# Optimization experiments

Hardware: AMD Instinct MI355X
Metric: run time of the kernel (lower is better)

The kernel has to match this reference:

```python
import jax, jax.numpy as jnp
import numpy as np

N_ATOMS = 16384
N_BLOCKS = 4096
K = 3          # top-k nearest context atoms (min(3, n_ctx) in original; n_ctx >> 3 here)
EPS_W = 1e-8   # inverse-distance weight epsilon (matches original)
EPS_D = 1e-12  # tiny epsilon inside sqrt for numerical safety of the distance


def setup_inputs() -> dict:
    key = jax.random.key(0)
    k1, k2, k3, k4, k5 = jax.random.split(key, 5)
    # coordinates spread out like real molecular coords (Angstrom-ish scale)
    X = jax.random.normal(k1, (N_ATOMS, 3), dtype=jnp.float32) * 10.0
    base_noise = jax.random.normal(k2, (N_ATOMS, 3), dtype=jnp.float32)      # randn_like(X)
    centroid_noise = jax.random.normal(k3, (N_ATOMS, 3), dtype=jnp.float32)  # per-atom randn(3)
    block_ids = jnp.sort(jax.random.randint(k4, (N_ATOMS,), 0, N_BLOCKS)).astype(jnp.int32)
    generate_mask = jax.random.randint(k5, (N_BLOCKS,), 0, 2).astype(bool)
    return {
        "X": X,
        "base_noise": base_noise,
        "centroid_noise": centroid_noise,
        "block_ids": block_ids,
        "generate_mask": generate_mask,
    }


def reference(X, base_noise, centroid_noise, block_ids, generate_mask):
    """Vectorized sample_chemical_prior: for every generated atom, find the 3
    nearest CONTEXT atoms, take an inverse-distance-weighted centroid, and add
    0.5 * gaussian noise. Non-generated atoms keep base_noise (randn_like)."""
    n = X.shape[0]
    gen_atoms = generate_mask[block_ids]           # [N] atoms being generated
    ctx = ~gen_atoms                               # [N] context atoms

    # pairwise squared distances via ||a||^2 + ||b||^2 - 2 a.b  -> [N, N]
    xn = jnp.sum(X * X, axis=-1)
    sq = xn[:, None] + xn[None, :] - 2.0 * (X @ X.T)
    d = jnp.sqrt(jnp.maximum(sq, 0.0) + EPS_D)

    # only context atoms are valid neighbor candidates; exclude self for safety
    not_self = ~jnp.eye(n, dtype=bool)
    d = jnp.where(ctx[None, :] & not_self, d, jnp.inf)

    # k nearest context atoms per row (smallest distances)
    neg_dk, idx = jax.lax.top_k(-d, K)             # [N, K]
    dk = -neg_dk

    # inverse-distance weights, normalized (matches original)
    w = 1.0 / (dk + EPS_W)
    w = w / jnp.sum(w, axis=-1, keepdims=True)

    coords = X[idx]                                # [N, K, 3] gather neighbor coords
    centroid = jnp.sum(coords * w[..., None], axis=1)  # [N, 3]

    x0 = jnp.where(gen_atoms[:, None], centroid + 0.5 * centroid_noise, base_noise)
    return x0
```

## Files before the change

### kernel.cpp

```cpp
#include <hip/hip_runtime.h>
#include <cstdint>

#define N_ATOMS 16384
#define NBLK 64
#define NTHR 256
#define G 24
#define NCELLS 13824
#define NCELLS_PAD 14336
#define CPT 14
#define BOX_LO -48.0f
#define INV_CELL 0.25f
#define SINIT 3.0e38f

#define OFF_COUNTS 0
#define OFF_ACELL 256
#define OFF_START 33280
#define OFF_GENIDX 90880
#define OFF_CTX4 156672

__device__ __forceinline__ int cell1(float x) {
    int c = (int)floorf((x - BOX_LO) * INV_CELL);
    return min(max(c, 0), G - 1);
}

__device__ __forceinline__ void ins3(float v, int vi,
                                     float& s1, float& s2, float& s3,
                                     int& i1, int& i2, int& i3)
{
    const bool b1 = v < s1, b2 = v < s2, b3 = v < s3;
    s3 = b2 ? s2 : (b3 ? v : s3);   i3 = b2 ? i2 : (b3 ? vi : i3);
    s2 = b1 ? s1 : (b2 ? v : s2);   i2 = b1 ? i1 : (b2 ? vi : i2);
    s1 = b1 ? v : s1;               i1 = b1 ? vi : i1;
}

__global__ __launch_bounds__(NTHR)
void k1_classify(const float* __restrict__ X,
                 const int* __restrict__ block_ids,
                 const unsigned int* __restrict__ mask,
                 const float* __restrict__ base_noise,
                 float* __restrict__ out,
                 unsigned short* __restrict__ acell)
{
    __shared__ int sflag;
    const int t = threadIdx.x;

    if (t == 0) sflag = 0;
    __syncthreads();
    if (mask[t] > 1u) sflag = 1;
    __syncthreads();
    const bool is_u8 = (sflag != 0);
    const unsigned char* m8 = (const unsigned char*)mask;

    const int i = blockIdx.x * NTHR + t;
    const int bid = block_ids[i];
    const bool g = is_u8 ? (m8[bid] != 0) : (mask[bid] != 0u);

    out[3 * i + 0] = base_noise[3 * i + 0];
    out[3 * i + 1] = base_noise[3 * i + 1];
    out[3 * i + 2] = base_noise[3 * i + 2];

    unsigned short c = 0xFFFFu;
    if (!g) {
        const float x = X[3 * i], y = X[3 * i + 1], z = X[3 * i + 2];
        c = (unsigned short)((cell1(z) * G + cell1(y)) * G + cell1(x));
    }
    acell[i] = c;
}

__global__ __launch_bounds__(1024)
void k2_sortscatter(const float* __restrict__ X,
                    const unsigned short* __restrict__ acell,
                    int* __restrict__ cell_start,
                    int* __restrict__ counts,
                    int* __restrict__ genidx,
                    float4* __restrict__ ctx4s)
{
    __shared__ int hist[NCELLS_PAD];
    __shared__ int wsum[16], wexc[16];
    const int t = threadIdx.x;
    const int wave = t >> 6, lane = t & 63;

    #pragma unroll
    for (int k = 0; k < CPT; ++k) hist[t * CPT + k] = 0;
    __syncthreads();

    #pragma unroll
    for (int it = 0; it < N_ATOMS / 1024; ++it) {
        const int i = it * 1024 + t;
        const unsigned short c = acell[i];
        const int bin = (c == 0xFFFFu) ? (NCELLS + ((i >> 8) & 63)) : (int)c;
        atomicAdd(&hist[bin], 1);
    }
    __syncthreads();

    int loc[CPT]; int sum = 0;
    #pragma unroll
    for (int k = 0; k < CPT; ++k) {
        const int v = hist[t * CPT + k];
        loc[k] = sum; sum += v;
    }
    int v = sum;
    #pragma unroll
    for (int d = 1; d < 64; d <<= 1) { const int u = __shfl_up(v, d); if (lane >= d) v += u; }
    if (lane == 63) wsum[wave] = v;
    __syncthreads();
    if (t < 16) {
        int v2 = wsum[t];
        const int orig = v2;
        #pragma unroll
        for (int d = 1; d < 16; d <<= 1) { const int u = __shfl_up(v2, d); if (t >= d) v2 += u; }
        wexc[t] = v2 - orig;
    }
    __syncthreads();
    const int base = wexc[wave] + (v - sum);
    #pragma unroll
    for (int k = 0; k < CPT; ++k) {
        const int st = base + loc[k];
        cell_start[t * CPT + k] = st;
        hist[t * CPT + k] = st;
    }
    if (t == 1023) cell_start[NCELLS_PAD] = base + sum;
    __syncthreads();

    const int nctx = hist[NCELLS];
    __syncthreads();

    #pragma unroll
    for (int it = 0; it < N_ATOMS / 1024; ++it) {
        const int i = it * 1024 + t;
        const unsigned short c = acell[i];
        const int bin = (c == 0xFFFFu) ? (NCELLS + ((i >> 8) & 63)) : (int)c;
        const int p = atomicAdd(&hist[bin], 1);
        if (c != 0xFFFFu) {
            const float x = X[3 * i], y = X[3 * i + 1], z = X[3 * i + 2];
            float xn = x * x; xn += y * y; xn += z * z;
            ctx4s[p] = make_float4(x, y, z, xn);
        } else {
            genidx[p - nctx] = i;
        }
    }
    if (t == 0) { counts[0] = nctx; counts[1] = N_ATOMS - nctx; }
}

#define P_X1(v)  __builtin_amdgcn_update_dpp(v, v, 0xB1, 0xF, 0xF, false)
#define P_X2(v)  __builtin_amdgcn_update_dpp(v, v, 0x4E, 0xF, 0xF, false)
#define P_R4(v)  __builtin_amdgcn_update_dpp(v, v, 0x124, 0xF, 0xF, false)
#define P_R8(v)  __builtin_amdgcn_update_dpp(v, v, 0x128, 0xF, 0xF, false)
#define P_S16(v) __builtin_amdgcn_ds_swizzle(v, 0x401F)
#define P_X32(v) __shfl_xor(v, 32)

__global__ __launch_bounds__(NTHR)
void k4_search(const float* __restrict__ X,
               const float* __restrict__ cnoise,
               const int* __restrict__ counts,
               const int* __restrict__ cell_start,
               const float4* __restrict__ ctx4s,
               const int* __restrict__ genidx,
               float* __restrict__ out)
{
    const int n_gen = counts[1];
    const int wave = threadIdx.x >> 6, lane = threadIdx.x & 63;
    if ((int)blockIdx.x * 4 >= n_gen) return;
    const int slot = (int)blockIdx.x * 4 + wave;
    if (slot >= n_gen) return;

    const int ai = genidx[slot];
    const float qx = X[3 * ai], qy = X[3 * ai + 1], qz = X[3 * ai + 2];
    float xnq = qx * qx; xnq += qy * qy; xnq += qz * qz;
    const int cqx = cell1(qx), cqy = cell1(qy), cqz = cell1(qz);

    float s1 = SINIT, s2 = SINIT, s3 = SINIT;
    int i1 = 0, i2 = 0, i3 = 0;

    {
        int st = 0, cnt = 0;
        if (lane < 9) {
            const int dy = lane % 3 - 1, dz = lane / 3 - 1;
            const int cy = cqy + dy, cz = cqz + dz;
            if ((unsigned)cy < G && (unsigned)cz < G) {
                const int xlo = max(cqx - 1, 0), xhi = min(cqx + 1, G - 1);
                const int c0 = (cz * G + cy) * G + xlo;
                st = cell_start[c0];
                cnt = cell_start[c0 + (xhi - xlo + 1)] - st;
            }
        }
        int stv[9], base[10];
        base[0] = 0;
        #pragma unroll
        for (int k = 0; k < 9; ++k) {
            stv[k] = __builtin_amdgcn_readlane(st, k);
            base[k + 1] = base[k] + __builtin_amdgcn_readlane(cnt, k);
        }
        const int T = base[9];
        const int nro = (T + 63) >> 6;
        if (nro > 0) {
            auto calcP = [&](int j) -> int {
                const int jc = min(j, T - 1);
                int p = stv[0] + jc;
                #pragma unroll
                for (int k = 1; k < 9; ++k)
                    p = (jc >= base[k]) ? stv[k] + (jc - base[k]) : p;
                return p;
            };
            int p0 = calcP(lane);
            float4 cc0 = ctx4s[p0];
            for (int ro = 0; ro < nro; ++ro) {
                int p1 = p0; float4 cc1 = cc0;
                if (ro + 1 < nro) { p1 = calcP((ro + 1) * 64 + lane); cc1 = ctx4s[p1]; }
                if (ro * 64 + lane < T) {
                    const float dot = qx * cc0.x + qy * cc0.y + qz * cc0.z;
                    const float sq = (xnq + cc0.w) - 2.0f * dot;
                    ins3(sq, p0, s1, s2, s3, i1, i2, i3);
                }
                p0 = p1; cc0 = cc1;
            }
        }
    }

    auto converged = [&](float bnd) -> bool {
        const int c = __popcll(__ballot(s1 + 0.01f < bnd))
                    + __popcll(__ballot(s2 + 0.01f < bnd))
                    + __popcll(__ballot(s3 + 0.01f < bnd));
        return c >= 3;
    };

    bool done = converged(16.0f);

    if (!done) {
        {
            const int P = 1, R = 2;
            const int B = 2 * R + 1;
            const int RP = R - P;
            const int PP = 2 * P + 1;
            const int A = 2 * RP * B;
            const int C = PP * 2 * RP;
            const int NS = A + C + 2 * PP * PP;
            int st = 0, cnt = 0;
            if (lane < NS) {
                const int u = lane;
                int dy, dz, xlo, xhi;
                if (u < A) {
                    const int q = u / B, rdy = u - q * B;
                    dz = (q < RP) ? (-R + q) : (P + 1 + (q - RP));
                    dy = rdy - R;
                    xlo = cqx - R; xhi = cqx + R;
                } else if (u < A + C) {
                    const int v2 = u - A, W = 2 * RP;
                    const int q = v2 / W, w = v2 - q * W;
                    dz = -P + q;
                    dy = (w < RP) ? (-R + w) : (P + 1 + (w - RP));
                    xlo = cqx - R; xhi = cqx + R;
                } else {
                    const int v2 = u - A - C;
                    const int side = v2 & 1, v3 = v2 >> 1;
                    dy = v3 % PP - P; dz = v3 / PP - P;
                    if (side) { xlo = cqx + P + 1; xhi = cqx + R; }
                    else      { xlo = cqx - R;     xhi = cqx - P - 1; }
                }
                const int cy = cqy + dy, cz = cqz + dz;
                if ((unsigned)cy < G && (unsigned)cz < G) {
                    xlo = max(xlo, 0); xhi = min(xhi, G - 1);
                    if (xlo <= xhi) {
                        const int c0 = (cz * G + cy) * G + xlo;
                        st = cell_start[c0];
                        cnt = cell_start[c0 + (xhi - xlo + 1)] - st;
                    }
                }
            }
            int pre = cnt;
            #pragma unroll
            for (int d = 1; d < 64; d <<= 1) {
                const int u = __shfl_up(pre, d);
                if (lane >= d) pre += u;
            }
            const int T = __shfl(pre, 63);
            const int ebase = pre - cnt;
            const int pk = st - ebase;
            const int iters = (T + 63) >> 6;
            for (int it = 0; it < iters; ++it) {
                const int j = it * 64 + lane;
                const int jc = min(j, T - 1);
                int L = 0;
                #pragma unroll
                for (int stp = 32; stp >= 1; stp >>= 1) {
                    const int cand = L + stp;
                    const int bv = __shfl(ebase, cand);
                    if (bv <= jc) L = cand;
                }
                const int p = __shfl(pk, L) + jc;
                const float4 cc = ctx4s[p];
                if (j < T) {
                    const float dot = qx * cc.x + qy * cc.y + qz * cc.z;
                    const float sq = (xnq + cc.w) - 2.0f * dot;
                    ins3(sq, p, s1, s2, s3, i1, i2, i3);
                }
            }
        }
        done = converged(64.0f);

        if (!done) {
            s1 = SINIT; s2 = SINIT; s3 = SINIT;
            i1 = 0; i2 = 0; i3 = 0;
            const int n_ctx = counts[0];
            for (int base = 0; base < n_ctx; base += 512) {
                const int pa0 = min(base + 0 * 64 + lane, n_ctx - 1);
                const int pa1 = min(base + 1 * 64 + lane, n_ctx - 1);
                const int pa2 = min(base + 2 * 64 + lane, n_ctx - 1);
                const int pa3 = min(base + 3 * 64 + lane, n_ctx - 1);
                const int pa4 = min(base + 4 * 64 + lane, n_ctx - 1);
                const int pa5 = min(base + 5 * 64 + lane, n_ctx - 1);
                const int pa6 = min(base + 6 * 64 + lane, n_ctx - 1);
                const int pa7 = min(base + 7 * 64 + lane, n_ctx - 1);
                const float4 cv0 = ctx4s[pa0], cv1 = ctx4s[pa1];
                const float4 cv2 = ctx4s[pa2], cv3 = ctx4s[pa3];
                const float4 cv4 = ctx4s[pa4], cv5 = ctx4s[pa5];
                const float4 cv6 = ctx4s[pa6], cv7 = ctx4s[pa7];
                #define TAIL_INS(K, CV, PA) \
                    if (base + (K) * 64 + lane < n_ctx) { \
                        const float dot = qx * (CV).x + qy * (CV).y + qz * (CV).z; \
                        const float sq = (xnq + (CV).w) - 2.0f * dot; \
                        ins3(sq, (PA), s1, s2, s3, i1, i2, i3); \
                    }
                TAIL_INS(0, cv0, pa0) TAIL_INS(1, cv1, pa1)
                TAIL_INS(2, cv2, pa2) TAIL_INS(3, cv3, pa3)
                TAIL_INS(4, cv4, pa4) TAIL_INS(5, cv5, pa5)
                TAIL_INS(6, cv6, pa6) TAIL_INS(7, cv7, pa7)
                #undef TAIL_INS
            }
        }
    }

    #define MERGE_STEP(PERM) { \
        const float a = __int_as_float(PERM(__float_as_int(s1))); const int ja = PERM(i1); \
        const float b = __int_as_float(PERM(__float_as_int(s2))); const int jb = PERM(i2); \
        const float c = __int_as_float(PERM(__float_as_int(s3))); const int jc = PERM(i3); \
        ins3(a, ja, s1, s2, s3, i1, i2, i3); \
        ins3(b, jb, s1, s2, s3, i1, i2, i3); \
        ins3(c, jc, s1, s2, s3, i1, i2, i3); }
    MERGE_STEP(P_X1)
    MERGE_STEP(P_X2)
    MERGE_STEP(P_R4)
    MERGE_STEP(P_R8)
    MERGE_STEP(P_S16)
    MERGE_STEP(P_X32)
    #undef MERGE_STEP

    if (lane == 0) {
        const float d1 = sqrtf(fmaxf(s1, 0.0f) + 1e-12f);
        const float d2 = sqrtf(fmaxf(s2, 0.0f) + 1e-12f);
        const float d3 = sqrtf(fmaxf(s3, 0.0f) + 1e-12f);
        float w1 = 1.0f / (d1 + 1e-8f);
        float w2 = 1.0f / (d2 + 1e-8f);
        float w3 = 1.0f / (d3 + 1e-8f);
        float wsum = w1 + w2;
        wsum += w3;
        w1 /= wsum; w2 /= wsum; w3 /= wsum;
        const float4 c1 = ctx4s[i1];
        const float4 c2 = ctx4s[i2];
        const float4 c3 = ctx4s[i3];
        float cxo = w1 * c1.x + w2 * c2.x; cxo += w3 * c3.x;
        float cyo = w1 * c1.y + w2 * c2.y; cyo += w3 * c3.y;
        float czo = w1 * c1.z + w2 * c2.z; czo += w3 * c3.z;
        out[3 * ai + 0] = cxo + 0.5f * cnoise[3 * ai + 0];
        out[3 * ai + 1] = cyo + 0.5f * cnoise[3 * ai + 1];
        out[3 * ai + 2] = czo + 0.5f * cnoise[3 * ai + 2];
    }
}

extern "C" void kernel_launch(void* const* d_in, const int* in_sizes, int n_in,
                              void* d_out, int out_size, void* d_ws, size_t ws_size,
                              hipStream_t stream) {
    const float* X          = (const float*)d_in[0];
    const float* base_noise = (const float*)d_in[1];
    const float* cnoise     = (const float*)d_in[2];
    const int*   block_ids  = (const int*)d_in[3];
    const unsigned int* gmask = (const unsigned int*)d_in[4];
    float* out = (float*)d_out;

    char* ws = (char*)d_ws;
    int*    counts     = (int*)(ws + OFF_COUNTS);
    unsigned short* acell = (unsigned short*)(ws + OFF_ACELL);
    int*    cell_start = (int*)(ws + OFF_START);
    int*    genidx     = (int*)(ws + OFF_GENIDX);
    float4* ctx4s      = (float4*)(ws + OFF_CTX4);

    k1_classify<<<NBLK, NTHR, 0, stream>>>(X, block_ids, gmask, base_noise,
                                           out, acell);
    k2_sortscatter<<<1, 1024, 0, stream>>>(X, acell, cell_start, counts,
                                           genidx, ctx4s);
    k4_search<<<N_ATOMS / 4, NTHR, 0, stream>>>(X, cnoise, counts, cell_start,
                                                ctx4s, genidx, out);
}
```

Before: 53.20 us.

## Split single-block sort-scatter into rank kernel plus parallel scatter kernel

```diff
diff --git a/kernel.cpp b/kernel.cpp
--- a/kernel.cpp
+++ b/kernel.cpp
@@ -13,10 +13,14 @@
 #define SINIT 3.0e38f
 
 #define OFF_COUNTS 0
-#define OFF_ACELL 256
-#define OFF_START 33280
-#define OFF_GENIDX 90880
-#define OFF_CTX4 156672
+#define OFF_BLKGEN 256
+#define OFF_BLKGOFF 512
+#define OFF_FLAGS 1024
+#define OFF_ACELL 3072
+#define OFF_POS 35840
+#define OFF_START 101376
+#define OFF_GENIDX 158976
+#define OFF_CTX4 224512
 
 __device__ __forceinline__ int cell1(float x) {
     int c = (int)floorf((x - BOX_LO) * INV_CELL);
@@ -39,10 +43,14 @@
                  const unsigned int* __restrict__ mask,
                  const float* __restrict__ base_noise,
                  float* __restrict__ out,
+                 unsigned long long* __restrict__ flags,
+                 int* __restrict__ blk_gen,
                  unsigned short* __restrict__ acell)
 {
     __shared__ int sflag;
+    __shared__ int wg[4];
     const int t = threadIdx.x;
+    const int wave = t >> 6, lane = t & 63;
 
     if (t == 0) sflag = 0;
     __syncthreads();
@@ -58,6 +66,11 @@
     out[3 * i + 0] = base_noise[3 * i + 0];
     out[3 * i + 1] = base_noise[3 * i + 1];
     out[3 * i + 2] = base_noise[3 * i + 2];
+
+    const unsigned long long mg = __ballot(g);
+    if (lane == 0) { flags[blockIdx.x * 4 + wave] = mg; wg[wave] = __popcll(mg); }
+    __syncthreads();
+    if (t == 0) blk_gen[blockIdx.x] = wg[0] + wg[1] + wg[2] + wg[3];
 
     unsigned short c = 0xFFFFu;
     if (!g) {
@@ -68,12 +81,12 @@
 }
 
 __global__ __launch_bounds__(1024)
-void k2_sortscatter(const float* __restrict__ X,
-                    const unsigned short* __restrict__ acell,
-                    int* __restrict__ cell_start,
-                    int* __restrict__ counts,
-                    int* __restrict__ genidx,
-                    float4* __restrict__ ctx4s)
+void k2_sort(const unsigned short* __restrict__ acell,
+             int* __restrict__ cell_start,
+             int* __restrict__ pos,
+             const int* __restrict__ blk_gen,
+             int* __restrict__ blk_goff,
+             int* __restrict__ counts)
 {
     __shared__ int hist[NCELLS_PAD];
     __shared__ int wsum[16], wexc[16];
@@ -86,10 +99,8 @@
 
     #pragma unroll
     for (int it = 0; it < N_ATOMS / 1024; ++it) {
-        const int i = it * 1024 + t;
-        const unsigned short c = acell[i];
-        const int bin = (c == 0xFFFFu) ? (NCELLS + ((i >> 8) & 63)) : (int)c;
-        atomicAdd(&hist[bin], 1);
+        const unsigned short c = acell[it * 1024 + t];
+        if (c != 0xFFFFu) atomicAdd(&hist[c], 1);
     }
     __syncthreads();
 
@@ -122,24 +133,50 @@
     if (t == 1023) cell_start[NCELLS_PAD] = base + sum;
     __syncthreads();
 
-    const int nctx = hist[NCELLS];
-    __syncthreads();
-
     #pragma unroll
     for (int it = 0; it < N_ATOMS / 1024; ++it) {
         const int i = it * 1024 + t;
         const unsigned short c = acell[i];
-        const int bin = (c == 0xFFFFu) ? (NCELLS + ((i >> 8) & 63)) : (int)c;
-        const int p = atomicAdd(&hist[bin], 1);
-        if (c != 0xFFFFu) {
-            const float x = X[3 * i], y = X[3 * i + 1], z = X[3 * i + 2];
-            float xn = x * x; xn += y * y; xn += z * z;
-            ctx4s[p] = make_float4(x, y, z, xn);
-        } else {
-            genidx[p - nctx] = i;
-        }
-    }
-    if (t == 0) { counts[0] = nctx; counts[1] = N_ATOMS - nctx; }
+        if (c != 0xFFFFu) pos[i] = atomicAdd(&hist[c], 1);
+    }
+
+    if (t < 64) {
+        const int o = blk_gen[t];
+        int s = o;
+        #pragma unroll
+        for (int d = 1; d < 64; d <<= 1) { const int u = __shfl_up(s, d); if (t >= d) s += u; }
+        blk_goff[t] = s - o;
+        if (t == 63) { counts[1] = s; counts[0] = N_ATOMS - s; }
+    }
+}
+
+__global__ __launch_bounds__(NTHR)
+void k3_scatter(const float* __restrict__ X,
+                const unsigned long long* __restrict__ flags,
+                const int* __restrict__ blk_goff,
+                const int* __restrict__ pos,
+                float4* __restrict__ ctx4s,
+                int* __restrict__ genidx)
+{
+    const int t = threadIdx.x;
+    const int wave = t >> 6, lane = t & 63;
+    const int i = blockIdx.x * NTHR + t;
+    const unsigned long long fw = flags[blockIdx.x * 4 + wave];
+    const bool g = (fw >> lane) & 1ull;
+    if (g) {
+        int og = blk_goff[blockIdx.x];
+        #pragma unroll
+        for (int w = 0; w < 4; ++w) {
+            if (w < wave) og += __popcll(flags[blockIdx.x * 4 + w]);
+        }
+        const unsigned long long below = (1ull << lane) - 1ull;
+        og += __popcll(fw & below);
+        genidx[og] = i;
+    } else {
+        const float x = X[3 * i], y = X[3 * i + 1], z = X[3 * i + 2];
+        float xn = x * x; xn += y * y; xn += z * z;
+        ctx4s[pos[i]] = make_float4(x, y, z, xn);
+    }
 }
 
 #define P_X1(v)  __builtin_amdgcn_update_dpp(v, v, 0xB1, 0xF, 0xF, false)
@@ -302,19 +339,13 @@
             s1 = SINIT; s2 = SINIT; s3 = SINIT;
             i1 = 0; i2 = 0; i3 = 0;
             const int n_ctx = counts[0];
-            for (int base = 0; base < n_ctx; base += 512) {
+            for (int base = 0; base < n_ctx; base += 256) {
                 const int pa0 = min(base + 0 * 64 + lane, n_ctx - 1);
                 const int pa1 = min(base + 1 * 64 + lane, n_ctx - 1);
                 const int pa2 = min(base + 2 * 64 + lane, n_ctx - 1);
                 const int pa3 = min(base + 3 * 64 + lane, n_ctx - 1);
-                const int pa4 = min(base + 4 * 64 + lane, n_ctx - 1);
-                const int pa5 = min(base + 5 * 64 + lane, n_ctx - 1);
-                const int pa6 = min(base + 6 * 64 + lane, n_ctx - 1);
-                const int pa7 = min(base + 7 * 64 + lane, n_ctx - 1);
                 const float4 cv0 = ctx4s[pa0], cv1 = ctx4s[pa1];
                 const float4 cv2 = ctx4s[pa2], cv3 = ctx4s[pa3];
-                const float4 cv4 = ctx4s[pa4], cv5 = ctx4s[pa5];
-                const float4 cv6 = ctx4s[pa6], cv7 = ctx4s[pa7];
                 #define TAIL_INS(K, CV, PA) \
                     if (base + (K) * 64 + lane < n_ctx) { \
                         const float dot = qx * (CV).x + qy * (CV).y + qz * (CV).z; \
@@ -323,8 +354,6 @@
                     }
                 TAIL_INS(0, cv0, pa0) TAIL_INS(1, cv1, pa1)
                 TAIL_INS(2, cv2, pa2) TAIL_INS(3, cv3, pa3)
-                TAIL_INS(4, cv4, pa4) TAIL_INS(5, cv5, pa5)
-                TAIL_INS(6, cv6, pa6) TAIL_INS(7, cv7, pa7)
                 #undef TAIL_INS
             }
         }
@@ -379,15 +408,19 @@
 
     char* ws = (char*)d_ws;
     int*    counts     = (int*)(ws + OFF_COUNTS);
+    int*    blk_gen    = (int*)(ws + OFF_BLKGEN);
+    int*    blk_goff   = (int*)(ws + OFF_BLKGOFF);
+    unsigned long long* flags = (unsigned long long*)(ws + OFF_FLAGS);
     unsigned short* acell = (unsigned short*)(ws + OFF_ACELL);
+    int*    pos        = (int*)(ws + OFF_POS);
     int*    cell_start = (int*)(ws + OFF_START);
     int*    genidx     = (int*)(ws + OFF_GENIDX);
     float4* ctx4s      = (float4*)(ws + OFF_CTX4);
 
     k1_classify<<<NBLK, NTHR, 0, stream>>>(X, block_ids, gmask, base_noise,
-                                           out, acell);
-    k2_sortscatter<<<1, 1024, 0, stream>>>(X, acell, cell_start, counts,
-                                           genidx, ctx4s);
+                                           out, flags, blk_gen, acell);
+    k2_sort<<<1, 1024, 0, stream>>>(acell, cell_start, pos, blk_gen, blk_goff, counts);
+    k3_scatter<<<NBLK, NTHR, 0, stream>>>(X, flags, blk_goff, pos, ctx4s, genidx);
     k4_search<<<N_ATOMS / 4, NTHR, 0, stream>>>(X, cnoise, counts, cell_start,
                                                 ctx4s, genidx, out);
 }
```

Measured after the change: 47.67 us. 1.12x faster.

## Split sort and scatter, pack gen/ctx counts into one histogram

Applied to the files above, without the earlier changes.

```diff
diff --git a/kernel.cpp b/kernel.cpp
--- a/kernel.cpp
+++ b/kernel.cpp
@@ -14,9 +14,10 @@
 
 #define OFF_COUNTS 0
 #define OFF_ACELL 256
-#define OFF_START 33280
-#define OFF_GENIDX 90880
-#define OFF_CTX4 156672
+#define OFF_POS 33280
+#define OFF_START 98816
+#define OFF_GENIDX 156416
+#define OFF_CTX4 222208
 
 __device__ __forceinline__ int cell1(float x) {
     int c = (int)floorf((x - BOX_LO) * INV_CELL);
@@ -59,21 +60,18 @@
     out[3 * i + 1] = base_noise[3 * i + 1];
     out[3 * i + 2] = base_noise[3 * i + 2];
 
-    unsigned short c = 0xFFFFu;
-    if (!g) {
-        const float x = X[3 * i], y = X[3 * i + 1], z = X[3 * i + 2];
-        c = (unsigned short)((cell1(z) * G + cell1(y)) * G + cell1(x));
-    }
+    const float x = X[3 * i], y = X[3 * i + 1], z = X[3 * i + 2];
+    const unsigned short c =
+        (unsigned short)(((cell1(z) * G + cell1(y)) * G + cell1(x)) |
+                         (g ? 0x8000 : 0));
     acell[i] = c;
 }
 
 __global__ __launch_bounds__(1024)
-void k2_sortscatter(const float* __restrict__ X,
-                    const unsigned short* __restrict__ acell,
-                    int* __restrict__ cell_start,
-                    int* __restrict__ counts,
-                    int* __restrict__ genidx,
-                    float4* __restrict__ ctx4s)
+void k2_sort(const unsigned short* __restrict__ acell,
+             int* __restrict__ cell_start,
+             int* __restrict__ pos,
+             int* __restrict__ counts)
 {
     __shared__ int hist[NCELLS_PAD];
     __shared__ int wsum[16], wexc[16];
@@ -86,10 +84,10 @@
 
     #pragma unroll
     for (int it = 0; it < N_ATOMS / 1024; ++it) {
-        const int i = it * 1024 + t;
-        const unsigned short c = acell[i];
-        const int bin = (c == 0xFFFFu) ? (NCELLS + ((i >> 8) & 63)) : (int)c;
-        atomicAdd(&hist[bin], 1);
+        const unsigned short c = acell[it * 1024 + t];
+        const int bin = c & 0x3FFF;
+        const int inc = (c & 0x8000) ? 65536 : 1;
+        atomicAdd(&hist[bin], inc);
     }
     __syncthreads();
 
@@ -116,30 +114,45 @@
     #pragma unroll
     for (int k = 0; k < CPT; ++k) {
         const int st = base + loc[k];
-        cell_start[t * CPT + k] = st;
+        cell_start[t * CPT + k] = st & 0xFFFF;
         hist[t * CPT + k] = st;
     }
-    if (t == 1023) cell_start[NCELLS_PAD] = base + sum;
-    __syncthreads();
-
-    const int nctx = hist[NCELLS];
+    if (t == 1023) {
+        const int tot = base + sum;
+        cell_start[NCELLS_PAD] = tot & 0xFFFF;
+        counts[0] = tot & 0xFFFF;
+        counts[1] = tot >> 16;
+    }
     __syncthreads();
 
     #pragma unroll
     for (int it = 0; it < N_ATOMS / 1024; ++it) {
         const int i = it * 1024 + t;
         const unsigned short c = acell[i];
-        const int bin = (c == 0xFFFFu) ? (NCELLS + ((i >> 8) & 63)) : (int)c;
-        const int p = atomicAdd(&hist[bin], 1);
-        if (c != 0xFFFFu) {
-            const float x = X[3 * i], y = X[3 * i + 1], z = X[3 * i + 2];
-            float xn = x * x; xn += y * y; xn += z * z;
-            ctx4s[p] = make_float4(x, y, z, xn);
-        } else {
-            genidx[p - nctx] = i;
-        }
-    }
-    if (t == 0) { counts[0] = nctx; counts[1] = N_ATOMS - nctx; }
+        const int bin = c & 0x3FFF;
+        const int inc = (c & 0x8000) ? 65536 : 1;
+        const int old = atomicAdd(&hist[bin], inc);
+        pos[i] = (c & 0x8000) ? (old >> 16) : (old & 0xFFFF);
+    }
+}
+
+__global__ __launch_bounds__(NTHR)
+void k3_scatter(const float* __restrict__ X,
+                const unsigned short* __restrict__ acell,
+                const int* __restrict__ pos,
+                float4* __restrict__ ctx4s,
+                int* __restrict__ genidx)
+{
+    const int t = threadIdx.x;
+    const int i = blockIdx.x * NTHR + t;
+    const unsigned short c = acell[i];
+    if (c & 0x8000) {
+        genidx[pos[i]] = i;
+    } else {
+        const float x = X[3 * i], y = X[3 * i + 1], z = X[3 * i + 2];
+        float xn = x * x; xn += y * y; xn += z * z;
+        ctx4s[pos[i]] = make_float4(x, y, z, xn);
+    }
 }
 
 #define P_X1(v)  __builtin_amdgcn_update_dpp(v, v, 0xB1, 0xF, 0xF, false)
@@ -302,19 +315,13 @@
             s1 = SINIT; s2 = SINIT; s3 = SINIT;
             i1 = 0; i2 = 0; i3 = 0;
             const int n_ctx = counts[0];
-            for (int base = 0; base < n_ctx; base += 512) {
+            for (int base = 0; base < n_ctx; base += 256) {
                 const int pa0 = min(base + 0 * 64 + lane, n_ctx - 1);
                 const int pa1 = min(base + 1 * 64 + lane, n_ctx - 1);
                 const int pa2 = min(base + 2 * 64 + lane, n_ctx - 1);
                 const int pa3 = min(base + 3 * 64 + lane, n_ctx - 1);
-                const int pa4 = min(base + 4 * 64 + lane, n_ctx - 1);
-                const int pa5 = min(base + 5 * 64 + lane, n_ctx - 1);
-                const int pa6 = min(base + 6 * 64 + lane, n_ctx - 1);
-                const int pa7 = min(base + 7 * 64 + lane, n_ctx - 1);
                 const float4 cv0 = ctx4s[pa0], cv1 = ctx4s[pa1];
                 const float4 cv2 = ctx4s[pa2], cv3 = ctx4s[pa3];
-                const float4 cv4 = ctx4s[pa4], cv5 = ctx4s[pa5];
-                const float4 cv6 = ctx4s[pa6], cv7 = ctx4s[pa7];
                 #define TAIL_INS(K, CV, PA) \
                     if (base + (K) * 64 + lane < n_ctx) { \
                         const float dot = qx * (CV).x + qy * (CV).y + qz * (CV).z; \
@@ -323,8 +330,6 @@
                     }
                 TAIL_INS(0, cv0, pa0) TAIL_INS(1, cv1, pa1)
                 TAIL_INS(2, cv2, pa2) TAIL_INS(3, cv3, pa3)
-                TAIL_INS(4, cv4, pa4) TAIL_INS(5, cv5, pa5)
-                TAIL_INS(6, cv6, pa6) TAIL_INS(7, cv7, pa7)
                 #undef TAIL_INS
             }
         }
@@ -380,14 +385,15 @@
     char* ws = (char*)d_ws;
     int*    counts     = (int*)(ws + OFF_COUNTS);
     unsigned short* acell = (unsigned short*)(ws + OFF_ACELL);
+    int*    pos        = (int*)(ws + OFF_POS);
     int*    cell_start = (int*)(ws + OFF_START);
     int*    genidx     = (int*)(ws + OFF_GENIDX);
     float4* ctx4s      = (float4*)(ws + OFF_CTX4);
 
     k1_classify<<<NBLK, NTHR, 0, stream>>>(X, block_ids, gmask, base_noise,
                                            out, acell);
-    k2_sortscatter<<<1, 1024, 0, stream>>>(X, acell, cell_start, counts,
-                                           genidx, ctx4s);
+    k2_sort<<<1, 1024, 0, stream>>>(acell, cell_start, pos, counts);
+    k3_scatter<<<NBLK, NTHR, 0, stream>>>(X, acell, pos, ctx4s, genidx);
     k4_search<<<N_ATOMS / 4, NTHR, 0, stream>>>(X, cnoise, counts, cell_start,
                                                 ctx4s, genidx, out);
 }
```

Result: faster. 47.62 us (-10.5%).
